# Optimization experiments

Measured on AMD Instinct MI355X. Metric: run time of the kernel, lower is better.

The kernel has to match this reference:

```python
import jax, jax.numpy as jnp
import numpy as np


def _pos_encoding(seq_len, d_model, dtype):
    # Faithful to the original: exponent uses dim itself (not dim-1 for odd dims).
    dims = jnp.arange(d_model, dtype=dtype)                     # [D]
    positions = jnp.arange(seq_len, dtype=dtype)                # [S]
    inv_freq = jnp.power(jnp.asarray(10000.0, dtype), dims / d_model)  # [D]
    angle = positions[:, None] / inv_freq[None, :]              # [S, D]
    even = (jnp.arange(d_model) % 2) == 0                       # [D]
    return jnp.where(even[None, :], jnp.sin(angle), jnp.cos(angle))  # [S, D]


def setup_inputs() -> dict:
    key = jax.random.key(0)
    x = jax.random.normal(key, (8, 4096, 1024), dtype=jnp.float32)
    return {"x": x}


def reference(x) -> jnp.ndarray:
    B, S, D = x.shape
    enc = _pos_encoding(S, D, x.dtype)  # [S, D]
    # Dropout in eval mode is identity, so output is x + encoding.
    return x + enc[None, :, :]
```

## Files before the change

### kernel.cpp

```cpp
#include <hip/hip_runtime.h>
#include <math.h>


#define S_LEN 4096
#define D_LEN 1024

typedef float f32x4 __attribute__((ext_vector_type(4)));

#define NF4_ROW   256
#define TSTRIDE   (2048 * 256)
#define NITER     16

__global__ __launch_bounds__(256) void pe_add_kernel(
    const float* __restrict__ x, float* __restrict__ out, int B) {
    const int t = blockIdx.x * 256 + threadIdx.x;

    const float c = -9.210340371976184f / (float)D_LEN;

    if (B == 8) {
        const int col = t & (NF4_ROW - 1);
        const int r0  = t >> 8;
        const int d0  = col << 2;

        const float f0 = expf((float)(d0 + 0) * c);
        const float f1 = expf((float)(d0 + 1) * c);
        const float f2 = expf((float)(d0 + 2) * c);
        const float f3 = expf((float)(d0 + 3) * c);

        const float sa = (float)r0;
        const float sb = (float)(r0 + 2048);

        f32x4 ea, eb;
        ea.x = sinf(sa * f0); ea.y = cosf(sa * f1);
        ea.z = sinf(sa * f2); ea.w = cosf(sa * f3);
        eb.x = sinf(sb * f0); eb.y = cosf(sb * f1);
        eb.z = sinf(sb * f2); eb.w = cosf(sb * f3);

        const f32x4* px = (const f32x4*)x + t;
        f32x4*       po = (f32x4*)out + t;

        #pragma unroll 4
        for (int k = 0; k < NITER; ++k) {
            f32x4 v = *px;
            v += (k & 1) ? eb : ea;
            __builtin_nontemporal_store(v, po);
            px += TSTRIDE;
            po += TSTRIDE;
        }
    } else {
        const size_t nf4 = (size_t)B * S_LEN * (D_LEN / 4);
        for (size_t i = t; i < nf4; i += (size_t)TSTRIDE) {
            const int col = (int)(i & (NF4_ROW - 1));
            const int s   = (int)((i / NF4_ROW) % S_LEN);
            const int d0  = col << 2;
            const float sf = (float)s;
            f32x4 e;
            e.x = sinf(sf * expf((float)(d0 + 0) * c));
            e.y = cosf(sf * expf((float)(d0 + 1) * c));
            e.z = sinf(sf * expf((float)(d0 + 2) * c));
            e.w = cosf(sf * expf((float)(d0 + 3) * c));
            f32x4 v = ((const f32x4*)x)[i];
            v += e;
            ((f32x4*)out)[i] = v;
        }
    }
}

extern "C" void kernel_launch(void* const* d_in, const int* in_sizes, int n_in,
                              void* d_out, int out_size, void* d_ws, size_t ws_size,
                              hipStream_t stream) {
    const float* x = (const float*)d_in[0];
    float* out = (float*)d_out;
    const int B = in_sizes[0] / (S_LEN * D_LEN);

    dim3 grid(2048);
    dim3 block(256);
    pe_add_kernel<<<grid, block, 0, stream>>>(x, out, B);
}
```

Baseline: 235.2 us.

## Issue all batch loads up front via inline asm, one row per thread

Each thread now covers a single sequence row across all 8 batches instead of two rows across 16 iterations, and the grid doubles to 4096 blocks. The 8 global loads are issued back to back with inline asm, and a `s_waitcnt vmcnt(7)` before each add lets it start as soon as its own load lands. This keeps more memory requests in flight per thread. Stores become ordinary stores instead of nontemporal ones. The hand-written waitcnt relies on loads and stores retiring in order on this hardware and on the counter accounting being exact, so it is fragile.

```diff
diff --git a/kernel.cpp b/kernel.cpp
--- a/kernel.cpp
+++ b/kernel.cpp
@@ -7,10 +7,6 @@
 
 typedef float f32x4 __attribute__((ext_vector_type(4)));
 
-#define NF4_ROW   256
-#define TSTRIDE   (2048 * 256)
-#define NITER     16
-
 __global__ __launch_bounds__(256) void pe_add_kernel(
     const float* __restrict__ x, float* __restrict__ out, int B) {
     const int t = blockIdx.x * 256 + threadIdx.x;
@@ -18,42 +14,44 @@
     const float c = -9.210340371976184f / (float)D_LEN;
 
     if (B == 8) {
-        const int col = t & (NF4_ROW - 1);
-        const int r0  = t >> 8;
+        const int col = t & 255;
+        const int s   = t >> 8;
         const int d0  = col << 2;
+        const float sf = (float)s;
 
-        const float f0 = expf((float)(d0 + 0) * c);
-        const float f1 = expf((float)(d0 + 1) * c);
-        const float f2 = expf((float)(d0 + 2) * c);
-        const float f3 = expf((float)(d0 + 3) * c);
+        f32x4 e;
+        e.x = sinf(sf * expf((float)(d0 + 0) * c));
+        e.y = cosf(sf * expf((float)(d0 + 1) * c));
+        e.z = sinf(sf * expf((float)(d0 + 2) * c));
+        e.w = cosf(sf * expf((float)(d0 + 3) * c));
 
-        const float sa = (float)r0;
-        const float sb = (float)(r0 + 2048);
+        const unsigned int voff = (unsigned int)t << 4;
 
-        f32x4 ea, eb;
-        ea.x = sinf(sa * f0); ea.y = cosf(sa * f1);
-        ea.z = sinf(sa * f2); ea.w = cosf(sa * f3);
-        eb.x = sinf(sb * f0); eb.y = cosf(sb * f1);
-        eb.z = sinf(sb * f2); eb.w = cosf(sb * f3);
+        f32x4 v0, v1, v2, v3, v4, v5, v6, v7;
+        #define LOADK(vk, k)                                                  \
+            asm volatile("global_load_dwordx4 %0, %1, %2"                     \
+                         : "=v"(vk)                                           \
+                         : "v"(voff), "s"(x + ((size_t)(k) << 22))            \
+                         : "memory")
+        LOADK(v0, 0); LOADK(v1, 1); LOADK(v2, 2); LOADK(v3, 3);
+        LOADK(v4, 4); LOADK(v5, 5); LOADK(v6, 6); LOADK(v7, 7);
+        #undef LOADK
 
-        const f32x4* px = (const f32x4*)x + t;
-        f32x4*       po = (f32x4*)out + t;
-
-        #pragma unroll 4
-        for (int k = 0; k < NITER; ++k) {
-            f32x4 v = *px;
-            v += (k & 1) ? eb : ea;
-            __builtin_nontemporal_store(v, po);
-            px += TSTRIDE;
-            po += TSTRIDE;
-        }
+        f32x4* o = (f32x4*)out;
+        #define STEPK(vk, k)                                                  \
+            asm volatile("s_waitcnt vmcnt(7)" : "+v"(vk) :: "memory");        \
+            vk += e;                                                          \
+            o[((size_t)(k) << 20) + (size_t)t] = vk
+        STEPK(v0, 0); STEPK(v1, 1); STEPK(v2, 2); STEPK(v3, 3);
+        STEPK(v4, 4); STEPK(v5, 5); STEPK(v6, 6); STEPK(v7, 7);
+        #undef STEPK
     } else {
         const size_t nf4 = (size_t)B * S_LEN * (D_LEN / 4);
-        for (size_t i = t; i < nf4; i += (size_t)TSTRIDE) {
-            const int col = (int)(i & (NF4_ROW - 1));
-            const int s   = (int)((i / NF4_ROW) % S_LEN);
-            const int d0  = col << 2;
-            const float sf = (float)s;
+        for (size_t i = t; i < nf4; i += (size_t)4096 * 256) {
+            const int col = (int)(i & 255);
+            const int srow = (int)((i >> 8) & (S_LEN - 1));
+            const int d0 = col << 2;
+            const float sf = (float)srow;
             f32x4 e;
             e.x = sinf(sf * expf((float)(d0 + 0) * c));
             e.y = cosf(sf * expf((float)(d0 + 1) * c));
@@ -73,7 +71,7 @@
     float* out = (float*)d_out;
     const int B = in_sizes[0] / (S_LEN * D_LEN);
 
-    dim3 grid(2048);
+    dim3 grid(4096);
     dim3 block(256);
     pe_add_kernel<<<grid, block, 0, stream>>>(x, out, B);
 }
```

After: 244.2 us. +3.8%, slower.
